# Optimization experiments

Measured on AMD Instinct MI355X. Metric: run time of the kernel, lower is better.

Reference implementation:

```python
import jax, jax.numpy as jnp
import numpy as np

N_V, N_G, K, C_IN, DW, NB, E = 8192, 4096, 128, 128, 64, 4, 65536
SIGMA, CUT = 4.0, 8.0


def setup_inputs() -> dict:
    key = jax.random.key(0)
    ks = iter(jax.random.split(key, 64))
    s = 0.05
    def rn(shape):
        return jax.random.normal(next(ks), shape, dtype=jnp.float32) * s
    p = {}
    p['vertices'] = jax.random.uniform(next(ks), (N_V, 3), dtype=jnp.float32) * 30.0
    p['graph_pos'] = jax.random.uniform(next(ks), (N_G, 3), dtype=jnp.float32) * 30.0
    p['x_in'] = jax.random.normal(next(ks), (N_V, C_IN), dtype=jnp.float32)
    p['graph_x'] = jax.random.normal(next(ks), (N_G, C_IN), dtype=jnp.float32)
    p['mass'] = jax.random.uniform(next(ks), (N_V,), dtype=jnp.float32) + 0.5
    p['evals'] = jax.random.uniform(next(ks), (K,), dtype=jnp.float32) * 10.0
    p['evecs'] = jax.random.normal(next(ks), (N_V, K), dtype=jnp.float32) * 0.011
    p['gradX'] = jax.random.normal(next(ks), (N_V, N_V), dtype=jnp.float32) * 0.01
    p['gradY'] = jax.random.normal(next(ks), (N_V, N_V), dtype=jnp.float32) * 0.01
    p['graph_edge_index'] = jax.random.randint(next(ks), (2, E), 0, N_G)
    p['graph_edge_weight'] = jax.random.uniform(next(ks), (E,), dtype=jnp.float32)
    p['lin1_w'] = rn((C_IN, DW)); p['lin1_b'] = rn((DW,))
    p['lin2_w'] = rn((C_IN, DW)); p['lin2_b'] = rn((DW,))
    p['diff_time'] = jax.random.uniform(next(ks), (NB, DW), dtype=jnp.float32) * 0.5 + 0.01
    p['A_re'] = rn((NB, DW, DW)); p['A_im'] = rn((NB, DW, DW))
    p['mlp_w0'] = rn((NB, 3 * DW, DW)); p['mlp_b0'] = rn((NB, DW))
    p['mlp_w1'] = rn((NB, DW, DW)); p['mlp_b1'] = rn((NB, DW))
    p['mlp_w2'] = rn((NB, DW, DW)); p['mlp_b2'] = rn((NB, DW))
    p['gcn1_w'] = rn((NB, DW, DW)); p['gcn1_b'] = rn((NB, DW))
    p['gcn2_w'] = rn((NB, DW, DW)); p['gcn2_b'] = rn((NB, DW))
    p['gs_w'] = rn((NB, DW, DW)); p['gs_b'] = rn((NB, DW))
    p['sg_w'] = rn((NB, DW, DW)); p['sg_b'] = rn((NB, DW))
    return p


def _gcn_conv(x, src, dst, ew, W, b, n):
    # PyG GCNConv with self-loops (fill 1.0): D^-1/2 (A+I) D^-1/2 (x W) + b
    xw = x @ W
    deg = jnp.ones((n,), xw.dtype).at[dst].add(ew)
    dinv = 1.0 / jnp.sqrt(deg)
    norm = dinv[src] * ew * dinv[dst]
    agg = jnp.zeros_like(xw).at[dst].add(norm[:, None] * xw[src])
    return agg + xw / deg[:, None] + b


def _forward(vertices, graph_pos, x_in, graph_x, mass, evals, evecs, gradX, gradY,
             graph_edge_weight, lin1_w, lin1_b, lin2_w, lin2_b, diff_time, A_re, A_im,
             mlp_w0, mlp_b0, mlp_w1, mlp_b1, mlp_w2, mlp_b2,
             gcn1_w, gcn1_b, gcn2_w, gcn2_b, gs_w, gs_b, sg_w, sg_b, graph_edge_index):
    n_v = vertices.shape[0]
    # torch.cdist + cutoff + exp(-d/sigma), under no_grad in the original
    d = jnp.sqrt(jnp.maximum(jnp.sum((vertices[:, None, :] - graph_pos[None, :, :]) ** 2, -1), 0.0))
    Wb = jax.lax.stop_gradient(jnp.where(d < CUT, jnp.exp(-d / SIGMA), 0.0))  # [n_v, n_g]
    deg_v = 1.0 + Wb.sum(1)  # vertex in-degree incl. self-loop (graphsurf direction)
    deg_g = 1.0 + Wb.sum(0)  # graph-node in-degree incl. self-loop (surfgraph direction)
    rsv = 1.0 / jnp.sqrt(deg_v)
    rsg = 1.0 / jnp.sqrt(deg_g)
    src, dst = graph_edge_index[0], graph_edge_index[1]
    diff_x = x_in @ lin1_w + lin1_b
    gx = graph_x @ lin2_w + lin2_b
    n_g = gx.shape[0]
    for i in range(NB):
        # --- DiffusionNet block (spectral) ---
        t = jnp.maximum(diff_time[i], 1e-8)
        spec = evecs.T @ (diff_x * mass[:, None])              # [K, DW]
        xd = evecs @ (jnp.exp(-evals[:, None] * t[None, :]) * spec)
        gX = gradX @ xd                                         # real part of gradient
        gY = gradY @ xd                                         # imag part of gradient
        br = gX @ A_re[i] - gY @ A_im[i]
        bi = gY @ A_re[i] + gX @ A_im[i]
        gf = jnp.tanh(gX * br + gY * bi)                        # spatial gradient features
        h = jnp.concatenate([diff_x, xd, gf], axis=-1)
        h = jax.nn.relu(h @ mlp_w0[i] + mlp_b0[i])
        h = jax.nn.relu(h @ mlp_w1[i] + mlp_b1[i])
        diff_x = diff_x + h @ mlp_w2[i] + mlp_b2[i]
        # --- internal graph GCN (eval mode: dropout = identity) ---
        gx = jax.nn.relu(_gcn_conv(gx, src, dst, graph_edge_weight, gcn1_w[i], gcn1_b[i], n_g))
        gx = _gcn_conv(gx, src, dst, graph_edge_weight, gcn2_w[i], gcn2_b[i], n_g)
        # --- bipartite GCNConvs on concatenated nodes ---
        xall = jnp.concatenate([diff_x, gx], axis=0)
        xw = xall @ gs_w[i]   # graphsurf: graph -> surface edges
        os_v = xw[:n_v] / deg_v[:, None] + (Wb @ xw[n_v:]) * rsv[:, None] + gs_b[i]
        os_g = xw[n_v:] + gs_b[i]
        xw2 = xall @ sg_w[i]  # surfgraph: surface -> graph edges
        og_g = xw2[n_v:] / deg_g[:, None] + (Wb.T @ xw2[:n_v]) * rsg[:, None] + sg_b[i]
        og_v = xw2[:n_v] + sg_b[i]
        diff_x = 0.5 * (os_v + og_v)
        gx = 0.5 * (os_g + og_g)
    return diff_x  # [n_v, C_out]


def reference(vertices, graph_pos, x_in, graph_x, mass, evals, evecs, gradX, gradY,
              graph_edge_index, graph_edge_weight, lin1_w, lin1_b, lin2_w, lin2_b,
              diff_time, A_re, A_im, mlp_w0, mlp_b0, mlp_w1, mlp_b1, mlp_w2, mlp_b2,
              gcn1_w, gcn1_b, gcn2_w, gcn2_b, gs_w, gs_b, sg_w, sg_b):
    return _forward(vertices, graph_pos, x_in, graph_x, mass, evals, evecs, gradX, gradY,
                    graph_edge_weight, lin1_w, lin1_b, lin2_w, lin2_b, diff_time, A_re, A_im,
                    mlp_w0, mlp_b0, mlp_w1, mlp_b1, mlp_w2, mlp_b2,
                    gcn1_w, gcn1_b, gcn2_w, gcn2_b, gs_w, gs_b, sg_w, sg_b, graph_edge_index)
```

## Files before the change

kernel.cpp:

```cpp
#include <hip/hip_runtime.h>
#include <hip/hip_bf16.h>

typedef unsigned short u16;
typedef __attribute__((ext_vector_type(8))) short sh8;
typedef __attribute__((ext_vector_type(4))) float f32x4;

#define NV 8192
#define NG 4096
#define NE 65536
#define NSLICE 32

__device__ __forceinline__ u16 f2bf(float f) {
  __hip_bfloat16 h = __float2bfloat16(f);
  return __builtin_bit_cast(u16, h);
}

__device__ __forceinline__ void gl_lds16(const void* g, void* l) {
  __builtin_amdgcn_global_load_lds(
      (const __attribute__((address_space(1))) void*)g,
      (__attribute__((address_space(3))) void*)l, 16, 0, 0);
}

__global__ void k_fill4(float* __restrict__ deg_v, float* __restrict__ deg_g,
                        float* __restrict__ deg_e, int* __restrict__ cnt) {
  int i = blockIdx.x * 256 + threadIdx.x;
  if (i < NV) deg_v[i] = 1.f;
  int j = i - NV;
  if (j >= 0 && j < NG) deg_g[j] = 1.f;
  j -= NG;
  if (j >= 0 && j < NG) deg_e[j] = 1.f;
  j -= NG;
  if (j >= 0 && j < NG) cnt[j] = 0;
}

__global__ __launch_bounds__(256) void k_wb_build(
    const float* __restrict__ vert, const float* __restrict__ gpos,
    u16* __restrict__ WbRow, u16* __restrict__ WbP, u16* __restrict__ WbTP,
    float* __restrict__ deg_v, float* __restrict__ deg_g) {
  __shared__ float lv[192], lg[192], colp[256];
  __shared__ float tile[64][65];
  int t = threadIdx.x;
  int v0 = blockIdx.x * 64, g0 = blockIdx.y * 64;
  if (t < 192) { lv[t] = vert[(size_t)v0 * 3 + t]; lg[t] = gpos[(size_t)g0 * 3 + t]; }
  __syncthreads();
  int w = t >> 6, lane = t & 63;
  float gx_ = lg[lane * 3], gy_ = lg[lane * 3 + 1], gz_ = lg[lane * 3 + 2];
  float csum = 0.f;
  #pragma unroll 4
  for (int s = 0; s < 16; s++) {
    int vl = w + 4 * s;
    float dx = lv[vl * 3] - gx_, dy = lv[vl * 3 + 1] - gy_, dz = lv[vl * 3 + 2] - gz_;
    float d = sqrtf(dx * dx + dy * dy + dz * dz);
    float W = (d < 8.0f) ? expf(d * -0.25f) : 0.f;
    if (WbRow != nullptr) WbRow[(size_t)(v0 + vl) * NG + g0 + lane] = f2bf(W);
    tile[vl][lane] = W;
    csum += W;
  }
  colp[t] = csum;
  __syncthreads();
  int r4 = t >> 2, q = t & 3;
  float rs = 0.f;
  #pragma unroll
  for (int j = 0; j < 16; j++) rs += tile[r4][q * 16 + j];
  rs += __shfl_xor(rs, 1);
  rs += __shfl_xor(rs, 2);
  if (q == 0) atomicAdd(&deg_v[v0 + r4], rs);
  if (w == 0) {
    float tot = colp[lane] + colp[64 + lane] + colp[128 + lane] + colp[192 + lane];
    atomicAdd(&deg_g[g0 + lane], tot);
  }
  if (WbP != nullptr) {
    size_t tb = ((size_t)(v0 >> 7) * 64 + (g0 >> 6)) * 8192;
    #pragma unroll
    for (int j = 0; j < 2; j++) {
      int idx = j * 256 + t;
      int vr = idx >> 3, k8 = (idx & 7) * 8;
      u16 pk[8];
      #pragma unroll
      for (int qq = 0; qq < 8; qq++) pk[qq] = f2bf(tile[vr][k8 + qq]);
      int r = (v0 & 64) + vr;
      *(uint4*)&WbP[tb + (size_t)r * 64 + (size_t)(((k8 >> 3) ^ (r & 7)) << 3)] = *(uint4*)pk;
    }
  }
  if (WbTP != nullptr) {
    size_t tb = ((size_t)(g0 >> 7) * 128 + (v0 >> 6)) * 8192;
    #pragma unroll
    for (int j = 0; j < 2; j++) {
      int idx = j * 256 + t;
      int gr = idx >> 3, v8 = (idx & 7) * 8;
      u16 pk[8];
      #pragma unroll
      for (int qq = 0; qq < 8; qq++) pk[qq] = f2bf(tile[v8 + qq][gr]);
      int r = (g0 & 64) + gr;
      *(uint4*)&WbTP[tb + (size_t)r * 64 + (size_t)(((v8 >> 3) ^ (r & 7)) << 3)] = *(uint4*)pk;
    }
  }
}

__global__ void k_recips(const float* __restrict__ deg_v, float* __restrict__ inv_v,
                         float* __restrict__ rs_v, const float* __restrict__ deg_g,
                         float* __restrict__ inv_g, float* __restrict__ rs_g,
                         const float* __restrict__ deg_e, float* __restrict__ inv_e,
                         float* __restrict__ rs_e) {
  int i = blockIdx.x * 256 + threadIdx.x;
  if (i < NV) { float d = deg_v[i]; inv_v[i] = 1.f / d; rs_v[i] = 1.f / sqrtf(d); }
  else if (i < NV + NG) {
    int j = i - NV; float d = deg_g[j]; inv_g[j] = 1.f / d; rs_g[j] = 1.f / sqrtf(d);
  } else if (i < NV + 2 * NG) {
    int j = i - NV - NG; float d = deg_e[j]; inv_e[j] = 1.f / d; rs_e[j] = 1.f / sqrtf(d);
  }
}

__global__ void k_edge_prep(const int* __restrict__ eidx, const float* __restrict__ ew,
                            float* __restrict__ deg_e, int* __restrict__ cnt) {
  int e = blockIdx.x * 256 + threadIdx.x;
  if (e < NE) { int d = eidx[NE + e]; atomicAdd(&deg_e[d], ew[e]); atomicAdd(&cnt[d], 1); }
}

__global__ __launch_bounds__(1024) void k_scan(const int* __restrict__ cnt,
    int* __restrict__ row_ptr, int* __restrict__ cursor) {
  __shared__ int buf0[1024], buf1[1024];
  int t = threadIdx.x;
  int b = t * 4;
  int c0 = cnt[b], c1 = cnt[b + 1], c2 = cnt[b + 2], c3 = cnt[b + 3];
  int s = c0 + c1 + c2 + c3;
  buf0[t] = s;
  __syncthreads();
  int* src = buf0; int* dst = buf1;
  for (int off = 1; off < 1024; off <<= 1) {
    int v = src[t];
    if (t >= off) v += src[t - off];
    dst[t] = v;
    __syncthreads();
    int* tmp = src; src = dst; dst = tmp;
  }
  int excl = (t == 0) ? 0 : src[t - 1];
  int r0 = excl, r1 = excl + c0, r2 = excl + c0 + c1, r3 = excl + c0 + c1 + c2;
  row_ptr[b] = r0; row_ptr[b + 1] = r1; row_ptr[b + 2] = r2; row_ptr[b + 3] = r3;
  cursor[b] = r0; cursor[b + 1] = r1; cursor[b + 2] = r2; cursor[b + 3] = r3;
  if (t == 1023) row_ptr[4096] = src[1023];
}

__global__ void k_scatter(const int* __restrict__ eidx, const float* __restrict__ ew,
                          const float* __restrict__ dinv, int* __restrict__ cursor,
                          int* __restrict__ csrc, float* __restrict__ cnorm) {
  int e = blockIdx.x * 256 + threadIdx.x;
  if (e < NE) {
    int s = eidx[e], d = eidx[NE + e];
    int slot = atomicAdd(&cursor[d], 1);
    csrc[slot] = s;
    cnorm[slot] = dinv[s] * ew[e] * dinv[d];
  }
}

__global__ __launch_bounds__(256) void k_evecsT(const float* __restrict__ ev, u16* __restrict__ evT) {
  __shared__ float tile[32][33];
  int t = threadIdx.x;
  int v0 = blockIdx.x * 32, k0 = blockIdx.y * 32;
  int r = t >> 3, c4 = (t & 7) * 4;
  float4 x = *(const float4*)(ev + (size_t)(v0 + r) * 128 + k0 + c4);
  tile[r][c4] = x.x; tile[r][c4 + 1] = x.y; tile[r][c4 + 2] = x.z; tile[r][c4 + 3] = x.w;
  __syncthreads();
  u16* dst = evT + (size_t)(k0 + r) * NV + v0 + c4;
  dst[0] = f2bf(tile[c4][r]); dst[1] = f2bf(tile[c4 + 1][r]);
  dst[2] = f2bf(tile[c4 + 2][r]); dst[3] = f2bf(tile[c4 + 3][r]);
}

__global__ __launch_bounds__(256) void gemm_setup2(
    const float* __restrict__ gXm, const float* __restrict__ gYm,
    const u16* __restrict__ evT, float* __restrict__ C2) {
  extern __shared__ __align__(16) char smem[];
  const int t = threadIdx.x;
  const int lane = t & 63, wave = t >> 6;
  const int rl = lane & 15, hi = lane >> 4;
  const int mat = blockIdx.x >> 7, mb = blockIdx.x & 127;
  const int m0 = mb * 64;
  const float* A = mat ? gYm : gXm;
  const int wm = (wave >> 1) * 32, wn = (wave & 1) * 64;

  f32x4 acc[2][4];
  #pragma unroll
  for (int a = 0; a < 2; a++)
    #pragma unroll
    for (int b = 0; b < 4; b++) acc[a][b] = f32x4{0.f, 0.f, 0.f, 0.f};

  auto STAGE = [&](int buf, int k0) {
    char* aB = smem + buf * 65536;
    #pragma unroll
    for (int jj = 0; jj < 8; jj++) {
      int j = wave * 8 + jj;
      int r = 2 * j + (lane >> 5);
      const float* src = A + (size_t)(m0 + r) * NV + k0 + (((lane & 31) ^ (r & 7)) << 2);
      gl_lds16(src, aB + j * 1024);
    }
    char* bB = aB + 32768;
    #pragma unroll
    for (int jj = 0; jj < 8; jj++) {
      int j = wave * 8 + jj;
      int n = 4 * j + (lane >> 4);
      const u16* srcb = evT + (size_t)n * NV + k0 + (((lane & 15) ^ (n & 7)) << 3);
      gl_lds16(srcb, bB + j * 1024);
    }
  };

  auto COMPUTE = [&](int buf) {
    const float* Af = (const float*)(smem + buf * 65536);
    const u16* Bf = (const u16*)(smem + buf * 65536 + 32768);
    #pragma unroll
    for (int step = 0; step < 4; step++) {
      sh8 av[2], bv[4];
      #pragma unroll
      for (int mf = 0; mf < 2; mf++) {
        int r = wm + mf * 16 + rl;
        int s0 = step * 8 + hi * 2;
        f32x4 lo = *(const f32x4*)(Af + r * 128 + ((s0 ^ (r & 7)) << 2));
        f32x4 hi4 = *(const f32x4*)(Af + r * 128 + (((s0 + 1) ^ (r & 7)) << 2));
        sh8 v;
        v[0] = (short)f2bf(lo[0]); v[1] = (short)f2bf(lo[1]);
        v[2] = (short)f2bf(lo[2]); v[3] = (short)f2bf(lo[3]);
        v[4] = (short)f2bf(hi4[0]); v[5] = (short)f2bf(hi4[1]);
        v[6] = (short)f2bf(hi4[2]); v[7] = (short)f2bf(hi4[3]);
        av[mf] = v;
      }
      #pragma unroll
      for (int nf = 0; nf < 4; nf++) {
        int n = wn + nf * 16 + rl;
        int s = step * 4 + hi;
        bv[nf] = *(const sh8*)(Bf + n * 128 + ((s ^ (n & 7)) << 3));
      }
      #pragma unroll
      for (int mf = 0; mf < 2; mf++)
        #pragma unroll
        for (int nf = 0; nf < 4; nf++)
          acc[mf][nf] = __builtin_amdgcn_mfma_f32_16x16x32_bf16(av[mf], bv[nf], acc[mf][nf], 0, 0, 0);
    }
  };

  STAGE(0, 0);
  STAGE(1, 128);
  for (int ti = 0; ti < 64; ti++) {
    if (ti + 1 < 64) { asm volatile("s_waitcnt vmcnt(16)" ::: "memory"); }
    else             { asm volatile("s_waitcnt vmcnt(0)" ::: "memory"); }
    __builtin_amdgcn_sched_barrier(0);
    __builtin_amdgcn_s_barrier();
    COMPUTE(ti & 1);
    __builtin_amdgcn_sched_barrier(0);
    __builtin_amdgcn_s_barrier();
    if (ti + 2 < 64) STAGE(ti & 1, (ti + 2) * 128);
  }

  float* C = C2 + (size_t)mat * NV * 128;
  #pragma unroll
  for (int mf = 0; mf < 2; mf++)
    #pragma unroll
    for (int nf = 0; nf < 4; nf++) {
      int row = m0 + wm + mf * 16 + hi * 4;
      int col = wn + nf * 16 + rl;
      #pragma unroll
      for (int q = 0; q < 4; q++)
        C[(size_t)(row + q) * 128 + col] = acc[mf][nf][q];
    }
}

__global__ __launch_bounds__(256) void gemm_panel(
    const u16* __restrict__ Apan, int KT, const u16* __restrict__ BT, int ldbt,
    float* __restrict__ parts, int M, int nz, int ktpz) {
  __shared__ __align__(16) char smem[49152];
  const int t = threadIdx.x;
  const int lane = t & 63, wave = t >> 6;
  const int rl = lane & 15, hi = lane >> 4;
  const int mb = blockIdx.x / nz, z = blockIdx.x % nz;
  const int kt0 = z * ktpz;
  const int wm = wave * 32;

  f32x4 acc[2][4];
  #pragma unroll
  for (int a = 0; a < 2; a++)
    #pragma unroll
    for (int b = 0; b < 4; b++) acc[a][b] = f32x4{0.f, 0.f, 0.f, 0.f};

  auto STAGE = [&](int buf, int kt) {
    char* aB = smem + buf * 24576;
    const u16* tbase = Apan + ((size_t)mb * KT + kt) * 8192;
    #pragma unroll
    for (int jj = 0; jj < 4; jj++) {
      int j = wave * 4 + jj;
      gl_lds16(tbase + j * 512 + lane * 8, aB + j * 1024);
    }
    char* bB = aB + 16384;
    #pragma unroll
    for (int jj = 0; jj < 2; jj++) {
      int j = wave * 2 + jj;
      int n = 8 * j + (lane >> 3);
      const u16* srcb = BT + (size_t)n * ldbt + kt * 64 + (((lane & 7) ^ (n & 7)) << 3);
      gl_lds16(srcb, bB + j * 1024);
    }
  };

  auto COMPUTE = [&](int buf) {
    const u16* Af = (const u16*)(smem + buf * 24576);
    const u16* Bf = Af + 8192;
    #pragma unroll
    for (int step = 0; step < 2; step++) {
      sh8 av[2], bv[4];
      int s = step * 4 + hi;
      #pragma unroll
      for (int mf = 0; mf < 2; mf++) {
        int r = wm + mf * 16 + rl;
        av[mf] = *(const sh8*)(Af + r * 64 + ((s ^ (r & 7)) << 3));
      }
      #pragma unroll
      for (int nf = 0; nf < 4; nf++) {
        int n = nf * 16 + rl;
        bv[nf] = *(const sh8*)(Bf + n * 64 + ((s ^ (n & 7)) << 3));
      }
      #pragma unroll
      for (int mf = 0; mf < 2; mf++)
        #pragma unroll
        for (int nf = 0; nf < 4; nf++)
          acc[mf][nf] = __builtin_amdgcn_mfma_f32_16x16x32_bf16(av[mf], bv[nf], acc[mf][nf], 0, 0, 0);
    }
  };

  STAGE(0, kt0);
  if (ktpz > 1) STAGE(1, kt0 + 1);
  for (int ti = 0; ti < ktpz; ti++) {
    if (ti + 1 < ktpz) { asm volatile("s_waitcnt vmcnt(6)" ::: "memory"); }
    else               { asm volatile("s_waitcnt vmcnt(0)" ::: "memory"); }
    __builtin_amdgcn_sched_barrier(0);
    __builtin_amdgcn_s_barrier();
    COMPUTE(ti & 1);
    __builtin_amdgcn_sched_barrier(0);
    __builtin_amdgcn_s_barrier();
    if (ti + 2 < ktpz) STAGE(ti & 1, kt0 + ti + 2);
  }

  float* C = parts + (size_t)z * M * 64;
  #pragma unroll
  for (int mf = 0; mf < 2; mf++)
    #pragma unroll
    for (int nf = 0; nf < 4; nf++) {
      int row = mb * 128 + wm + mf * 16 + hi * 4;
      int col = nf * 16 + rl;
      #pragma unroll
      for (int q = 0; q < 4; q++)
        C[(size_t)(row + q) * 64 + col] = acc[mf][nf][q];
    }
}

__global__ __launch_bounds__(256) void gemm_bf16(
    const u16* __restrict__ Ab, int lda, const u16* __restrict__ BT, int ldbt,
    float* __restrict__ parts, int M, int kchunk) {
  __shared__ __align__(16) char smem[49152];
  const int t = threadIdx.x;
  const int lane = t & 63, wave = t >> 6;
  const int m0 = blockIdx.x * 128;
  const int kbeg = blockIdx.z * kchunk;
  const int nt = kchunk >> 6;
  const int wm = (wave >> 1) * 64, wn = (wave & 1) * 32;
  const int arl = lane >> 3, asl = lane & 7;

  f32x4 acc[4][2];
  #pragma unroll
  for (int a = 0; a < 4; a++)
    #pragma unroll
    for (int b = 0; b < 2; b++) acc[a][b] = f32x4{0.f, 0.f, 0.f, 0.f};

  auto STAGE = [&](int buf, int k0) {
    char* base = smem + buf * 24576;
    #pragma unroll
    for (int j = 0; j < 4; j++) {
      int R0 = (wave * 4 + j) * 8;
      int r = R0 + arl;
      int gs = asl ^ (r & 7);
      gl_lds16(Ab + (size_t)(m0 + r) * lda + k0 + gs * 8, base + R0 * 128);
    }
    char* bb = base + 16384;
    #pragma unroll
    for (int j = 0; j < 2; j++) {
      int R0 = (wave * 2 + j) * 8;
      int r = R0 + arl;
      int gs = asl ^ (r & 7);
      gl_lds16(BT + (size_t)r * ldbt + k0 + gs * 8, bb + R0 * 128);
    }
  };

  auto COMPUTE = [&](int buf) {
    char* base = smem + buf * 24576;
    const u16* Af = (const u16*)base;
    const u16* Bf = (const u16*)(base + 16384);
    #pragma unroll
    for (int kk = 0; kk < 2; kk++) {
      sh8 av[4], bv[2];
      #pragma unroll
      for (int mf = 0; mf < 4; mf++) {
        int r = wm + mf * 16 + (lane & 15);
        int g = kk * 4 + (lane >> 4);
        av[mf] = *(const sh8*)(Af + r * 64 + (g ^ (r & 7)) * 8);
      }
      #pragma unroll
      for (int nf = 0; nf < 2; nf++) {
        int r = wn + nf * 16 + (lane & 15);
        int g = kk * 4 + (lane >> 4);
        bv[nf] = *(const sh8*)(Bf + r * 64 + (g ^ (r & 7)) * 8);
      }
      #pragma unroll
      for (int mf = 0; mf < 4; mf++)
        #pragma unroll
        for (int nf = 0; nf < 2; nf++)
          acc[mf][nf] = __builtin_amdgcn_mfma_f32_16x16x32_bf16(av[mf], bv[nf], acc[mf][nf], 0, 0, 0);
    }
  };

  STAGE(0, kbeg);
  if (nt > 1) STAGE(1, kbeg + 64);
  for (int ti = 0; ti < nt; ti++) {
    if (ti + 1 < nt) { asm volatile("s_waitcnt vmcnt(6)" ::: "memory"); }
    else             { asm volatile("s_waitcnt vmcnt(0)" ::: "memory"); }
    __builtin_amdgcn_sched_barrier(0);
    __builtin_amdgcn_s_barrier();
    COMPUTE(ti & 1);
    __builtin_amdgcn_sched_barrier(0);
    __builtin_amdgcn_s_barrier();
    if (ti + 2 < nt) STAGE(ti & 1, kbeg + (ti + 2) * 64);
  }

  float* C = parts + (size_t)blockIdx.z * M * 64;
  #pragma unroll
  for (int mf = 0; mf < 4; mf++)
    #pragma unroll
    for (int nf = 0; nf < 2; nf++) {
      int row = m0 + wm + mf * 16 + (lane >> 4) * 4;
      int col = wn + nf * 16 + (lane & 15);
      #pragma unroll
      for (int q = 0; q < 4; q++)
        C[(size_t)(row + q) * 64 + col] = acc[mf][nf][q];
    }
}

template<int BN, bool AF32, bool ATRANS>
__global__ __launch_bounds__(256) void gemm_k(
    const void* __restrict__ Aptr, const void* __restrict__ A2, int zsplit2,
    const u16* __restrict__ BT, float* __restrict__ Cpart,
    int M, int N, int lda, int ldbt, int kchunk) {
  constexpr int NF = BN / 32;
  __shared__ u16 lA[128 * 40];
  __shared__ u16 lB[BN * 40];
  const int t = threadIdx.x;
  const int m0 = blockIdx.x * 128, n0 = blockIdx.y * BN;
  const void* Ause = Aptr;
  int kz = blockIdx.z;
  if (A2 != nullptr && kz >= zsplit2) { Ause = A2; kz -= zsplit2; }
  const int kbeg = kz * kchunk;
  const int lane = t & 63, wave = t >> 6;
  const int wm = (wave >> 1) * 64, wn = (wave & 1) * (BN / 2);
  f32x4 zero = {0.f, 0.f, 0.f, 0.f};
  f32x4 acc[4][NF];
  #pragma unroll
  for (int a = 0; a < 4; a++)
    #pragma unroll
    for (int b = 0; b < NF; b++) acc[a][b] = zero;

  for (int k0 = kbeg; k0 < kbeg + kchunk; k0 += 32) {
    if constexpr (!ATRANS) {
      const int r = t >> 1, cc = (t & 1) * 16;
      const u16* A = (const u16*)Ause + (size_t)(m0 + r) * lda + k0 + cc;
      *(uint4*)&lA[r * 40 + cc] = *(const uint4*)A;
      *(uint4*)&lA[r * 40 + cc + 8] = *(const uint4*)(A + 8);
    } else {
      const int kl = t >> 3, mb = (t & 7) * 16;
      const u16* A = (const u16*)Ause + (size_t)(k0 + kl) * lda + m0 + mb;
      u16 vals[16];
      *(uint4*)&vals[0] = *(const uint4*)A;
      *(uint4*)&vals[8] = *(const uint4*)(A + 8);
      #pragma unroll
      for (int j = 0; j < 16; j++) lA[(mb + j) * 40 + kl] = vals[j];
    }
    if constexpr (BN == 64) {
      const int r = t >> 2, cc = (t & 3) * 8;
      const u16* B = BT + (size_t)(n0 + r) * ldbt + k0 + cc;
      *(uint4*)&lB[r * 40 + cc] = *(const uint4*)B;
    } else {
      const int r = t >> 1, cc = (t & 1) * 16;
      const u16* B = BT + (size_t)(n0 + r) * ldbt + k0 + cc;
      *(uint4*)&lB[r * 40 + cc] = *(const uint4*)B;
      *(uint4*)&lB[r * 40 + cc + 8] = *(const uint4*)(B + 8);
    }
    __syncthreads();
    sh8 af[4], bfv[NF];
    #pragma unroll
    for (int mf = 0; mf < 4; mf++)
      af[mf] = *(const sh8*)&lA[(wm + mf * 16 + (lane & 15)) * 40 + (lane >> 4) * 8];
    #pragma unroll
    for (int nf = 0; nf < NF; nf++)
      bfv[nf] = *(const sh8*)&lB[(wn + nf * 16 + (lane & 15)) * 40 + (lane >> 4) * 8];
    #pragma unroll
    for (int mf = 0; mf < 4; mf++)
      #pragma unroll
      for (int nf = 0; nf < NF; nf++)
        acc[mf][nf] = __builtin_amdgcn_mfma_f32_16x16x32_bf16(af[mf], bfv[nf], acc[mf][nf], 0, 0, 0);
    __syncthreads();
  }
  float* C = Cpart + (size_t)blockIdx.z * M * N;
  #pragma unroll
  for (int mf = 0; mf < 4; mf++)
    #pragma unroll
    for (int nf = 0; nf < NF; nf++) {
      const int row = m0 + wm + mf * 16 + (lane >> 4) * 4;
      const int col = n0 + wn + nf * 16 + (lane & 15);
      #pragma unroll
      for (int q = 0; q < 4; q++)
        C[(size_t)(row + q) * N + col] = acc[mf][nf][q];
    }
}

__global__ void k_reduce(const float* __restrict__ parts, float* __restrict__ dst, int len, int nz) {
  int i = (blockIdx.x * 256 + threadIdx.x) * 4;
  if (i >= len) return;
  float4 s = *(const float4*)(parts + i);
  for (int z = 1; z < nz; z++) {
    float4 v = *(const float4*)(parts + (size_t)z * len + i);
    s.x += v.x; s.y += v.y; s.z += v.z; s.w += v.w;
  }
  *(float4*)(dst + i) = s;
}

__global__ __launch_bounds__(256) void k_lin_both(const float* __restrict__ x_in,
    const float* __restrict__ graph_x, const float* __restrict__ W1,
    const float* __restrict__ b1, const float* __restrict__ W2,
    const float* __restrict__ b2, float* __restrict__ outV, float* __restrict__ outG) {
  __shared__ float lW[8192];
  __shared__ float lb[64];
  int bb = blockIdx.x;
  bool isV = bb < 2048;
  const float* W = isV ? W1 : W2;
  const float* bi = isV ? b1 : b2;
  const float* A = isV ? x_in : graph_x;
  float* out = isV ? outV : outG;
  int rb = isV ? bb : bb - 2048;
  int t = threadIdx.x;
  for (int i = t; i < 8192; i += 256) lW[i] = W[i];
  if (t < 64) lb[t] = bi[t];
  __syncthreads();
  int row = rb * 4 + (t >> 6), c = t & 63;
  const float* Ar = A + (size_t)row * 128;
  float acc = lb[c];
  #pragma unroll 8
  for (int k = 0; k < 128; k++) acc += Ar[k] * lW[k * 64 + c];
  out[(size_t)row * 64 + c] = acc;
}

__global__ __launch_bounds__(64) void k_spec_part(const float* __restrict__ evecs,
    const float* __restrict__ mass, const float* __restrict__ dx, float* __restrict__ sp) {
  int k = blockIdx.x, c = threadIdx.x;
  int v0 = blockIdx.y * 256;
  float a0 = 0, a1 = 0, a2 = 0, a3 = 0;
  for (int v = v0; v < v0 + 256; v += 4) {
    a0 += evecs[(size_t)(v + 0) * 128 + k] * mass[v + 0] * dx[(size_t)(v + 0) * 64 + c];
    a1 += evecs[(size_t)(v + 1) * 128 + k] * mass[v + 1] * dx[(size_t)(v + 1) * 64 + c];
    a2 += evecs[(size_t)(v + 2) * 128 + k] * mass[v + 2] * dx[(size_t)(v + 2) * 64 + c];
    a3 += evecs[(size_t)(v + 3) * 128 + k] * mass[v + 3] * dx[(size_t)(v + 3) * 64 + c];
  }
  sp[(size_t)blockIdx.y * 8192 + k * 64 + c] = (a0 + a1) + (a2 + a3);
}

__global__ void k_es(const float* __restrict__ sp, const float* __restrict__ evals,
                     const float* __restrict__ dt, float* __restrict__ Es) {
  int i = blockIdx.x * 256 + threadIdx.x;
  int k = i >> 6, c = i & 63;
  float s = 0.f;
  #pragma unroll 8
  for (int z = 0; z < NSLICE; z++) s += sp[(size_t)z * 8192 + i];
  Es[i] = expf(-evals[k] * fmaxf(dt[c], 1e-8f)) * s;
}

__global__ __launch_bounds__(256) void k_xdgf(const float* __restrict__ evecs,
    const float* __restrict__ GXE, const float* __restrict__ GYE,
    const float* __restrict__ Es, const float* __restrict__ Are,
    const float* __restrict__ Aim, float* __restrict__ xd, float* __restrict__ gf) {
  __shared__ float lE[8192];
  __shared__ float lr[4096], li[4096];
  __shared__ float lgx[256], lgy[256];
  int t = threadIdx.x;
  for (int i = t; i < 8192; i += 256) lE[i] = Es[i];
  for (int i = t; i < 4096; i += 256) { lr[i] = Are[i]; li[i] = Aim[i]; }
  __syncthreads();
  int wr = t >> 6, c = t & 63;
  int row = blockIdx.x * 4 + wr;
  const float* er = evecs + (size_t)row * 128;
  const float* xr = GXE + (size_t)row * 128;
  const float* yr = GYE + (size_t)row * 128;
  float a0 = 0, a1 = 0, a2 = 0;
  #pragma unroll 8
  for (int k = 0; k < 128; k++) {
    float s = lE[k * 64 + c];
    a0 += er[k] * s; a1 += xr[k] * s; a2 += yr[k] * s;
  }
  lgx[wr * 64 + c] = a1;
  lgy[wr * 64 + c] = a2;
  __syncthreads();
  float br = 0.f, bi = 0.f;
  #pragma unroll 8
  for (int k = 0; k < 64; k++) {
    float gx = lgx[wr * 64 + k], gy = lgy[wr * 64 + k];
    float ar = lr[k * 64 + c], ai = li[k * 64 + c];
    br += gx * ar - gy * ai;
    bi += gy * ar + gx * ai;
  }
  xd[(size_t)row * 64 + c] = a0;
  gf[(size_t)row * 64 + c] = tanhf(a1 * br + a2 * bi);
}

__global__ __launch_bounds__(256) void k_mlp0(const float* __restrict__ dx,
    const float* __restrict__ xd, const float* __restrict__ gf,
    const float* __restrict__ W0, const float* __restrict__ b0, float* __restrict__ h1) {
  __shared__ float lW[12288];
  __shared__ float lb[64];
  int t = threadIdx.x;
  for (int i = t; i < 12288; i += 256) lW[i] = W0[i];
  if (t < 64) lb[t] = b0[t];
  __syncthreads();
  int row = blockIdx.x * 4 + (t >> 6), c = t & 63;
  const float* a0 = dx + (size_t)row * 64;
  const float* a1 = xd + (size_t)row * 64;
  const float* a2 = gf + (size_t)row * 64;
  float acc = lb[c];
  #pragma unroll 8
  for (int k = 0; k < 64; k++) acc += a0[k] * lW[k * 64 + c];
  #pragma unroll 8
  for (int k = 0; k < 64; k++) acc += a1[k] * lW[(64 + k) * 64 + c];
  #pragma unroll 8
  for (int k = 0; k < 64; k++) acc += a2[k] * lW[(128 + k) * 64 + c];
  h1[(size_t)row * 64 + c] = fmaxf(acc, 0.f);
}

__global__ __launch_bounds__(256) void k_mlp12(const float* __restrict__ h1,
    const float* __restrict__ W1, const float* __restrict__ b1,
    const float* __restrict__ W2, const float* __restrict__ b2, float* __restrict__ dx) {
  __shared__ float l1[4096], l2[4096], lb1[64], lb2[64], lrow[256];
  int t = threadIdx.x;
  for (int i = t; i < 4096; i += 256) { l1[i] = W1[i]; l2[i] = W2[i]; }
  if (t < 64) lb1[t] = b1[t];
  else if (t < 128) lb2[t - 64] = b2[t - 64];
  __syncthreads();
  int wr = t >> 6, c = t & 63;
  int row = blockIdx.x * 4 + wr;
  const float* hr = h1 + (size_t)row * 64;
  float h2 = lb1[c];
  #pragma unroll 8
  for (int k = 0; k < 64; k++) h2 += hr[k] * l1[k * 64 + c];
  h2 = fmaxf(h2, 0.f);
  lrow[wr * 64 + c] = h2;
  __syncthreads();
  float o = lb2[c] + dx[(size_t)row * 64 + c];
  #pragma unroll 8
  for (int k = 0; k < 64; k++) o += lrow[wr * 64 + k] * l2[k * 64 + c];
  dx[(size_t)row * 64 + c] = o;
}

template<bool BIAS, bool RELU, bool RES>
__global__ __launch_bounds__(256) void k_mm64(const float* __restrict__ A,
    const float* __restrict__ W, const float* __restrict__ b,
    const float* __restrict__ res, float* __restrict__ out) {
  __shared__ float lW[4096];
  __shared__ float lb[64];
  int t = threadIdx.x;
  for (int i = t; i < 4096; i += 256) lW[i] = W[i];
  if constexpr (BIAS) { if (t < 64) lb[t] = b[t]; }
  __syncthreads();
  int row = blockIdx.x * 4 + (t >> 6), c = t & 63;
  const float* Ar = A + (size_t)row * 64;
  float acc = 0.f;
  #pragma unroll 8
  for (int k = 0; k < 64; k++) acc += Ar[k] * lW[k * 64 + c];
  if constexpr (BIAS) acc += lb[c];
  if constexpr (RES) acc += res[(size_t)row * 64 + c];
  if constexpr (RELU) acc = fmaxf(acc, 0.f);
  out[(size_t)row * 64 + c] = acc;
}

template<bool TP, bool TQ>
__global__ __launch_bounds__(256) void k_mm_dual(const float* __restrict__ A,
    const float* __restrict__ W1, const float* __restrict__ W2,
    float* __restrict__ P, float* __restrict__ Q,
    u16* __restrict__ PT, u16* __restrict__ QT, int R) {
  __shared__ float l1[4096], l2[4096];
  int t = threadIdx.x;
  for (int i = t; i < 4096; i += 256) { l1[i] = W1[i]; l2[i] = W2[i]; }
  __syncthreads();
  int row = blockIdx.x * 4 + (t >> 6), c = t & 63;
  const float* Ar = A + (size_t)row * 64;
  float p = 0.f, q = 0.f;
  #pragma unroll 8
  for (int k = 0; k < 64; k++) { float a = Ar[k]; p += a * l1[k * 64 + c]; q += a * l2[k * 64 + c]; }
  P[(size_t)row * 64 + c] = p;
  Q[(size_t)row * 64 + c] = q;
  if constexpr (TP) PT[(size_t)c * R + row] = f2bf(p);
  if constexpr (TQ) QT[(size_t)c * R + row] = f2bf(q);
}

__global__ __launch_bounds__(64) void k_aggmm(const float* __restrict__ xw,
    const int* __restrict__ rp, const int* __restrict__ csrc,
    const float* __restrict__ cnorm, const float* __restrict__ invdeg,
    const float* __restrict__ b1, const float* __restrict__ W2, float* __restrict__ out) {
  __shared__ float lrow[64];
  int g = blockIdx.x, c = threadIdx.x;
  float acc = xw[(size_t)g * 64 + c] * invdeg[g] + b1[c];
  int j1 = rp[g + 1];
  for (int j = rp[g]; j < j1; j++) acc += cnorm[j] * xw[(size_t)csrc[j] * 64 + c];
  acc = fmaxf(acc, 0.f);
  lrow[c] = acc;
  __syncthreads();
  float o = 0.f;
  #pragma unroll 8
  for (int k = 0; k < 64; k++) o += lrow[k] * W2[k * 64 + c];
  out[(size_t)g * 64 + c] = o;
}

__global__ __launch_bounds__(64) void k_aggdual(const float* __restrict__ xw,
    const int* __restrict__ rp, const int* __restrict__ csrc,
    const float* __restrict__ cnorm, const float* __restrict__ invdeg,
    const float* __restrict__ b2, const float* __restrict__ gsw,
    const float* __restrict__ sgw, float* __restrict__ xw_g,
    float* __restrict__ xw2_g, u16* __restrict__ xwgT) {
  __shared__ float lrow[64];
  int g = blockIdx.x, c = threadIdx.x;
  float acc = xw[(size_t)g * 64 + c] * invdeg[g] + b2[c];
  int j1 = rp[g + 1];
  for (int j = rp[g]; j < j1; j++) acc += cnorm[j] * xw[(size_t)csrc[j] * 64 + c];
  lrow[c] = acc;
  __syncthreads();
  float p = 0.f, q = 0.f;
  #pragma unroll 8
  for (int k = 0; k < 64; k++) {
    float r = lrow[k];
    p += r * gsw[k * 64 + c];
    q += r * sgw[k * 64 + c];
  }
  xw_g[(size_t)g * 64 + c] = p;
  xw2_g[(size_t)g * 64 + c] = q;
  xwgT[(size_t)c * NG + g] = f2bf(p);
}

__global__ void k_combine(const float* __restrict__ xw_v, const float* __restrict__ Wbp,
    const float* __restrict__ xw2_v, const float* __restrict__ xw_g,
    const float* __restrict__ WbTp, const float* __restrict__ xw2_g,
    const float* __restrict__ inv_deg_v, const float* __restrict__ rsv,
    const float* __restrict__ inv_deg_g, const float* __restrict__ rsg,
    const float* __restrict__ gsb, const float* __restrict__ sgb,
    float* __restrict__ dx, float* __restrict__ gx) {
  int idx = blockIdx.x * 256 + threadIdx.x;
  if (idx < NV * 64) {
    int v = idx >> 6, c = idx & 63;
    dx[idx] = 0.5f * (xw_v[idx] * inv_deg_v[v] + Wbp[idx] * rsv[v] + gsb[c] + xw2_v[idx] + sgb[c]);
  } else {
    int j = idx - NV * 64;
    int g = j >> 6, c = j & 63;
    gx[j] = 0.5f * (xw_g[j] + gsb[c] + xw2_g[j] * inv_deg_g[g] + WbTp[j] * rsg[g] + sgb[c]);
  }
}

extern "C" void kernel_launch(void* const* d_in, const int* in_sizes, int n_in,
                              void* d_out, int out_size, void* d_ws, size_t ws_size,
                              hipStream_t stream) {
  const float* vertices  = (const float*)d_in[0];
  const float* graph_pos = (const float*)d_in[1];
  const float* x_in      = (const float*)d_in[2];
  const float* graph_x   = (const float*)d_in[3];
  const float* mass      = (const float*)d_in[4];
  const float* evals     = (const float*)d_in[5];
  const float* evecs     = (const float*)d_in[6];
  const float* gradX     = (const float*)d_in[7];
  const float* gradY     = (const float*)d_in[8];
  const int*   eidx      = (const int*)d_in[9];
  const float* ew        = (const float*)d_in[10];
  const float* lin1_w    = (const float*)d_in[11];
  const float* lin1_b    = (const float*)d_in[12];
  const float* lin2_w    = (const float*)d_in[13];
  const float* lin2_b    = (const float*)d_in[14];
  const float* diff_time = (const float*)d_in[15];
  const float* A_re      = (const float*)d_in[16];
  const float* A_im      = (const float*)d_in[17];
  const float* mlp_w0    = (const float*)d_in[18];
  const float* mlp_b0    = (const float*)d_in[19];
  const float* mlp_w1    = (const float*)d_in[20];
  const float* mlp_b1    = (const float*)d_in[21];
  const float* mlp_w2    = (const float*)d_in[22];
  const float* mlp_b2    = (const float*)d_in[23];
  const float* gcn1_w    = (const float*)d_in[24];
  const float* gcn1_b    = (const float*)d_in[25];
  const float* gcn2_w    = (const float*)d_in[26];
  const float* gcn2_b    = (const float*)d_in[27];
  const float* gs_w      = (const float*)d_in[28];
  const float* gs_b      = (const float*)d_in[29];
  const float* sg_w      = (const float*)d_in[30];
  const float* sg_b      = (const float*)d_in[31];

  char* base = (char*)d_ws;
  size_t off = 0;
  auto alloc = [&](size_t nbytes) -> void* {
    void* p = base + off;
    off += (nbytes + 255) & ~(size_t)255;
    return p;
  };
  const size_t MBy = 1024 * 1024;
  u16*   evecsT  = (u16*)alloc((size_t)128 * NV * 2);
  float* GXE2    = (float*)alloc((size_t)2 * NV * 128 * 4);
  float* GXE     = GXE2;
  float* GYE     = GXE2 + (size_t)NV * 128;
  float* sp      = (float*)alloc((size_t)NSLICE * 8192 * 4);
  float* Es      = (float*)alloc(8192 * 4);
  float* diffx   = (float*)alloc((size_t)NV * 64 * 4);
  float* gxb     = (float*)alloc((size_t)NG * 64 * 4);
  float* xd      = (float*)alloc((size_t)NV * 64 * 4);
  float* gf      = (float*)alloc((size_t)NV * 64 * 4);
  float* h1      = (float*)alloc((size_t)NV * 64 * 4);
  float* xw_v    = (float*)alloc((size_t)NV * 64 * 4);
  float* xw2_v   = (float*)alloc((size_t)NV * 64 * 4);
  float* xw_g    = (float*)alloc((size_t)NG * 64 * 4);
  float* xw2_g   = (float*)alloc((size_t)NG * 64 * 4);
  float* xw1     = (float*)alloc((size_t)NG * 64 * 4);
  float* xw2k    = (float*)alloc((size_t)NG * 64 * 4);
  u16*   xwgT    = (u16*)alloc((size_t)64 * NG * 2);
  u16*   xw2vT   = (u16*)alloc((size_t)64 * NV * 2);
  float* Wbp     = (float*)alloc((size_t)NV * 64 * 4);
  float* WbTp    = (float*)alloc((size_t)NG * 64 * 4);
  float* deg_v   = (float*)alloc(NV * 4);
  float* inv_deg_v = (float*)alloc(NV * 4);
  float* rsv     = (float*)alloc(NV * 4);
  float* deg_g   = (float*)alloc(NG * 4);
  float* inv_deg_g = (float*)alloc(NG * 4);
  float* rsg     = (float*)alloc(NG * 4);
  float* deg_e   = (float*)alloc(NG * 4);
  float* invdeg_e = (float*)alloc(NG * 4);
  float* dinv_e  = (float*)alloc(NG * 4);
  int*   cnt     = (int*)alloc(NG * 4);
  int*   row_ptr = (int*)alloc((NG + 1) * 4);
  int*   cursor  = (int*)alloc(NG * 4);
  int*   csr_src = (int*)alloc(NE * 4);
  float* csr_norm = (float*)alloc(NE * 4);

  size_t avail = ws_size > off ? ws_size - off : 0;
  u16 *WbP = nullptr, *WbTP = nullptr, *WbRow = nullptr;
  float* parts;
  if (avail >= 146 * MBy) {
    WbP  = (u16*)alloc((size_t)NV * NG * 2);
    WbTP = (u16*)alloc((size_t)NG * NV * 2);
    parts = (float*)alloc(16 * MBy);
  } else if (avail >= 81 * MBy) {
    WbRow = (u16*)alloc((size_t)NV * NG * 2);
    parts = (float*)alloc(16 * MBy);
  } else {
    WbRow = (u16*)alloc((size_t)NV * NG * 2);
    parts = (float*)alloc(16 * MBy);
  }
  if (off > ws_size) return;

  dim3 B256(256);

  k_fill4<<<dim3(80), B256, 0, stream>>>(deg_v, deg_g, deg_e, cnt);
  k_wb_build<<<dim3(128, 64), B256, 0, stream>>>(vertices, graph_pos, WbRow, WbP, WbTP, deg_v, deg_g);
  k_edge_prep<<<dim3(256), B256, 0, stream>>>(eidx, ew, deg_e, cnt);
  k_recips<<<dim3(64), B256, 0, stream>>>(deg_v, inv_deg_v, rsv, deg_g, inv_deg_g, rsg,
                                          deg_e, invdeg_e, dinv_e);
  k_scan<<<dim3(1), dim3(1024), 0, stream>>>(cnt, row_ptr, cursor);
  k_scatter<<<dim3(256), B256, 0, stream>>>(eidx, ew, dinv_e, cursor, csr_src, csr_norm);
  k_evecsT<<<dim3(256, 4), B256, 0, stream>>>(evecs, evecsT);
  gemm_setup2<<<dim3(256), B256, 131072, stream>>>(gradX, gradY, evecsT, GXE2);
  k_lin_both<<<dim3(3072), B256, 0, stream>>>(x_in, graph_x, lin1_w, lin1_b, lin2_w, lin2_b, diffx, gxb);

  for (int i = 0; i < 4; i++) {
    const float* dtrow = diff_time + i * 64;
    k_spec_part<<<dim3(128, NSLICE), dim3(64), 0, stream>>>(evecs, mass, diffx, sp);
    k_es<<<dim3(32), B256, 0, stream>>>(sp, evals, dtrow, Es);
    k_xdgf<<<dim3(2048), B256, 0, stream>>>(evecs, GXE, GYE, Es, A_re + i * 4096, A_im + i * 4096, xd, gf);
    k_mlp0<<<dim3(2048), B256, 0, stream>>>(diffx, xd, gf, mlp_w0 + i * 12288, mlp_b0 + i * 64, h1);
    k_mlp12<<<dim3(2048), B256, 0, stream>>>(h1, mlp_w1 + i * 4096, mlp_b1 + i * 64,
        mlp_w2 + i * 4096, mlp_b2 + i * 64, diffx);
    k_mm64<false, false, false><<<dim3(1024), B256, 0, stream>>>(gxb, gcn1_w + i * 4096, nullptr, nullptr, xw1);
    k_aggmm<<<dim3(NG), dim3(64), 0, stream>>>(xw1, row_ptr, csr_src, csr_norm, invdeg_e,
        gcn1_b + i * 64, gcn2_w + i * 4096, xw2k);
    k_aggdual<<<dim3(NG), dim3(64), 0, stream>>>(xw2k, row_ptr, csr_src, csr_norm, invdeg_e,
        gcn2_b + i * 64, gs_w + i * 4096, sg_w + i * 4096, xw_g, xw2_g, xwgT);
    k_mm_dual<false, true><<<dim3(2048), B256, 0, stream>>>(diffx, gs_w + i * 4096, sg_w + i * 4096,
        xw_v, xw2_v, nullptr, xw2vT, NV);
    if (WbP != nullptr) {
      gemm_panel<<<dim3(64 * 8), B256, 0, stream>>>(WbP, 64, xwgT, NG, parts, NV, 8, 8);
      k_reduce<<<dim3(512), B256, 0, stream>>>(parts, Wbp, NV * 64, 8);
      gemm_panel<<<dim3(32 * 16), B256, 0, stream>>>(WbTP, 128, xw2vT, NV, parts, NG, 16, 8);
      k_reduce<<<dim3(256), B256, 0, stream>>>(parts, WbTp, NG * 64, 16);
    } else {
      gemm_bf16<<<dim3(64, 1, 8), B256, 0, stream>>>(WbRow, NG, xwgT, NG, parts, NV, 512);
      k_reduce<<<dim3(512), B256, 0, stream>>>(parts, Wbp, NV * 64, 8);
      gemm_k<64, false, true><<<dim3(32, 1, 16), B256, 0, stream>>>(
          WbRow, nullptr, 1 << 30, xw2vT, parts, NG, 64, NG, NV, 512);
      k_reduce<<<dim3(256), B256, 0, stream>>>(parts, WbTp, NG * 64, 16);
    }
    k_combine<<<dim3(3072), B256, 0, stream>>>(xw_v, Wbp, xw2_v, xw_g, WbTp, xw2_g,
        inv_deg_v, rsv, inv_deg_g, rsg, gs_b + i * 64, sg_b + i * 64, diffx, gxb);
  }

  hipMemcpyAsync(d_out, diffx, (size_t)NV * 64 * 4, hipMemcpyDeviceToDevice, stream);
}
```

Baseline: 1.070 ms.

## Split-K setup GEMM with larger tiles; move spectral projection onto MFMA GEMM

The setup GEMM (gradX/gradY times evecs) is rebuilt with 256x128 tiles and K=32 stages, split across zsu K-chunks, and its partial results are summed by a new reduce kernel. The intent is better MFMA reuse and more blocks in flight for a GEMM that is bound by fp32 streaming. The per-block spectral projection, previously a scalar fp32 loop over 32 slices, now transposes mass*diffx into bf16 and runs the existing gemm_bf16 with 64-way split-K plus a reduce. This adds kernel launches, partial-sum traffic, more workspace, and bf16 rounding in the spectral coefficients.

```diff
diff --git a/kernel.cpp b/kernel.cpp
--- a/kernel.cpp
+++ b/kernel.cpp
@@ -8,7 +8,6 @@
 #define NV 8192
 #define NG 4096
 #define NE 65536
-#define NSLICE 32
 
 __device__ __forceinline__ u16 f2bf(float f) {
   __hip_bfloat16 h = __float2bfloat16(f);
@@ -166,96 +165,122 @@
   dst[2] = f2bf(tile[c4 + 2][r]); dst[3] = f2bf(tile[c4 + 3][r]);
 }
 
-__global__ __launch_bounds__(256) void gemm_setup2(
+__global__ __launch_bounds__(256) void k_mdxT(const float* __restrict__ dx,
+    const float* __restrict__ mass, u16* __restrict__ mdxT) {
+  __shared__ float tile[64][65];
+  __shared__ float lm[64];
+  int t = threadIdx.x;
+  int v0 = blockIdx.x * 64;
+  if (t < 64) lm[t] = mass[v0 + t];
+  #pragma unroll
+  for (int i = 0; i < 16; i++) {
+    int idx = i * 256 + t;
+    int r = idx >> 6, c = idx & 63;
+    tile[r][c] = dx[(size_t)(v0 + r) * 64 + c];
+  }
+  __syncthreads();
+  int c = t >> 2;
+  #pragma unroll
+  for (int i = 0; i < 2; i++) {
+    int vq = (t & 3) * 16 + i * 8;
+    u16 pk[8];
+    #pragma unroll
+    for (int q = 0; q < 8; q++) pk[q] = f2bf(lm[vq + q] * tile[vq + q][c]);
+    *(uint4*)&mdxT[(size_t)c * NV + v0 + vq] = *(uint4*)pk;
+  }
+}
+
+__global__ __launch_bounds__(256) void gemm_setup3(
     const float* __restrict__ gXm, const float* __restrict__ gYm,
-    const u16* __restrict__ evT, float* __restrict__ C2) {
+    const u16* __restrict__ evT, float* __restrict__ parts,
+    int z, int kchunk) {
   extern __shared__ __align__(16) char smem[];
   const int t = threadIdx.x;
   const int lane = t & 63, wave = t >> 6;
   const int rl = lane & 15, hi = lane >> 4;
-  const int mat = blockIdx.x >> 7, mb = blockIdx.x & 127;
-  const int m0 = mb * 64;
+  int b = blockIdx.x;
+  const int zi = b % z; b /= z;
+  const int mb = b & 31;
+  const int mat = b >> 5;
   const float* A = mat ? gYm : gXm;
-  const int wm = (wave >> 1) * 32, wn = (wave & 1) * 64;
-
-  f32x4 acc[2][4];
-  #pragma unroll
-  for (int a = 0; a < 2; a++)
-    #pragma unroll
-    for (int b = 0; b < 4; b++) acc[a][b] = f32x4{0.f, 0.f, 0.f, 0.f};
+  const int m0 = mb * 256;
+  const int kbeg = zi * kchunk;
+  const int nt = kchunk >> 5;
+  const int wm = wave * 64;
+
+  f32x4 acc[4][8];
+  #pragma unroll
+  for (int a = 0; a < 4; a++)
+    #pragma unroll
+    for (int bb = 0; bb < 8; bb++) acc[a][bb] = f32x4{0.f, 0.f, 0.f, 0.f};
 
   auto STAGE = [&](int buf, int k0) {
-    char* aB = smem + buf * 65536;
+    char* aB = smem + buf * 40960;
     #pragma unroll
     for (int jj = 0; jj < 8; jj++) {
-      int j = wave * 8 + jj;
-      int r = 2 * j + (lane >> 5);
-      const float* src = A + (size_t)(m0 + r) * NV + k0 + (((lane & 31) ^ (r & 7)) << 2);
-      gl_lds16(src, aB + j * 1024);
-    }
-    char* bB = aB + 32768;
-    #pragma unroll
-    for (int jj = 0; jj < 8; jj++) {
-      int j = wave * 8 + jj;
-      int n = 4 * j + (lane >> 4);
-      const u16* srcb = evT + (size_t)n * NV + k0 + (((lane & 15) ^ (n & 7)) << 3);
-      gl_lds16(srcb, bB + j * 1024);
+      int R0 = wave * 64 + jj * 8;
+      int r = R0 + (lane >> 3);
+      int s = lane & 7;
+      gl_lds16(A + (size_t)(m0 + r) * NV + k0 + ((s ^ (r & 7)) << 2), aB + R0 * 128);
+    }
+    char* bB = smem + buf * 40960 + 32768;
+    #pragma unroll
+    for (int jj = 0; jj < 2; jj++) {
+      int R0 = wave * 32 + jj * 16;
+      int n = R0 + (lane >> 2);
+      int s = lane & 3;
+      gl_lds16(evT + (size_t)n * NV + k0 + ((s ^ ((n >> 1) & 3)) << 3), bB + R0 * 64);
     }
   };
 
   auto COMPUTE = [&](int buf) {
-    const float* Af = (const float*)(smem + buf * 65536);
-    const u16* Bf = (const u16*)(smem + buf * 65536 + 32768);
-    #pragma unroll
-    for (int step = 0; step < 4; step++) {
-      sh8 av[2], bv[4];
-      #pragma unroll
-      for (int mf = 0; mf < 2; mf++) {
-        int r = wm + mf * 16 + rl;
-        int s0 = step * 8 + hi * 2;
-        f32x4 lo = *(const f32x4*)(Af + r * 128 + ((s0 ^ (r & 7)) << 2));
-        f32x4 hi4 = *(const f32x4*)(Af + r * 128 + (((s0 + 1) ^ (r & 7)) << 2));
-        sh8 v;
-        v[0] = (short)f2bf(lo[0]); v[1] = (short)f2bf(lo[1]);
-        v[2] = (short)f2bf(lo[2]); v[3] = (short)f2bf(lo[3]);
-        v[4] = (short)f2bf(hi4[0]); v[5] = (short)f2bf(hi4[1]);
-        v[6] = (short)f2bf(hi4[2]); v[7] = (short)f2bf(hi4[3]);
-        av[mf] = v;
-      }
-      #pragma unroll
-      for (int nf = 0; nf < 4; nf++) {
-        int n = wn + nf * 16 + rl;
-        int s = step * 4 + hi;
-        bv[nf] = *(const sh8*)(Bf + n * 128 + ((s ^ (n & 7)) << 3));
-      }
-      #pragma unroll
-      for (int mf = 0; mf < 2; mf++)
-        #pragma unroll
-        for (int nf = 0; nf < 4; nf++)
-          acc[mf][nf] = __builtin_amdgcn_mfma_f32_16x16x32_bf16(av[mf], bv[nf], acc[mf][nf], 0, 0, 0);
-    }
+    const float* Af = (const float*)(smem + buf * 40960);
+    const u16* Bf = (const u16*)(smem + buf * 40960 + 32768);
+    sh8 av[4], bv[8];
+    #pragma unroll
+    for (int mf = 0; mf < 4; mf++) {
+      int r = wm + mf * 16 + rl;
+      f32x4 lo = *(const f32x4*)(Af + r * 32 + (((2 * hi) ^ (r & 7)) << 2));
+      f32x4 h4 = *(const f32x4*)(Af + r * 32 + (((2 * hi + 1) ^ (r & 7)) << 2));
+      sh8 v;
+      v[0] = (short)f2bf(lo[0]); v[1] = (short)f2bf(lo[1]);
+      v[2] = (short)f2bf(lo[2]); v[3] = (short)f2bf(lo[3]);
+      v[4] = (short)f2bf(h4[0]); v[5] = (short)f2bf(h4[1]);
+      v[6] = (short)f2bf(h4[2]); v[7] = (short)f2bf(h4[3]);
+      av[mf] = v;
+    }
+    #pragma unroll
+    for (int nf = 0; nf < 8; nf++) {
+      int n = nf * 16 + rl;
+      bv[nf] = *(const sh8*)(Bf + n * 32 + ((hi ^ ((n >> 1) & 3)) << 3));
+    }
+    #pragma unroll
+    for (int mf = 0; mf < 4; mf++)
+      #pragma unroll
+      for (int nf = 0; nf < 8; nf++)
+        acc[mf][nf] = __builtin_amdgcn_mfma_f32_16x16x32_bf16(av[mf], bv[nf], acc[mf][nf], 0, 0, 0);
   };
 
-  STAGE(0, 0);
-  STAGE(1, 128);
-  for (int ti = 0; ti < 64; ti++) {
-    if (ti + 1 < 64) { asm volatile("s_waitcnt vmcnt(16)" ::: "memory"); }
+  STAGE(0, kbeg);
+  if (nt > 1) STAGE(1, kbeg + 32);
+  for (int ti = 0; ti < nt; ti++) {
+    if (ti + 1 < nt) { asm volatile("s_waitcnt vmcnt(10)" ::: "memory"); }
     else             { asm volatile("s_waitcnt vmcnt(0)" ::: "memory"); }
     __builtin_amdgcn_sched_barrier(0);
     __builtin_amdgcn_s_barrier();
     COMPUTE(ti & 1);
     __builtin_amdgcn_sched_barrier(0);
     __builtin_amdgcn_s_barrier();
-    if (ti + 2 < 64) STAGE(ti & 1, (ti + 2) * 128);
-  }
-
-  float* C = C2 + (size_t)mat * NV * 128;
-  #pragma unroll
-  for (int mf = 0; mf < 2; mf++)
-    #pragma unroll
-    for (int nf = 0; nf < 4; nf++) {
+    if (ti + 2 < nt) STAGE(ti & 1, kbeg + (ti + 2) * 32);
+  }
+
+  float* C = parts + (size_t)(mat * z + zi) * (NV * 128);
+  #pragma unroll
+  for (int mf = 0; mf < 4; mf++)
+    #pragma unroll
+    for (int nf = 0; nf < 8; nf++) {
       int row = m0 + wm + mf * 16 + hi * 4;
-      int col = wn + nf * 16 + rl;
+      int col = nf * 16 + rl;
       #pragma unroll
       for (int q = 0; q < 4; q++)
         C[(size_t)(row + q) * 128 + col] = acc[mf][nf][q];
@@ -525,6 +550,19 @@
   *(float4*)(dst + i) = s;
 }
 
+__global__ void k_reduce2(const float* __restrict__ parts, float* __restrict__ dst, int len, int nz) {
+  int i = (blockIdx.x * 256 + threadIdx.x) * 4;
+  if (i >= 2 * len) return;
+  int mat = i / len, j = i - mat * len;
+  const float* src = parts + (size_t)mat * nz * len + j;
+  float4 s = *(const float4*)src;
+  for (int z = 1; z < nz; z++) {
+    float4 v = *(const float4*)(src + (size_t)z * len);
+    s.x += v.x; s.y += v.y; s.z += v.z; s.w += v.w;
+  }
+  *(float4*)(dst + i) = s;
+}
+
 __global__ __launch_bounds__(256) void k_lin_both(const float* __restrict__ x_in,
     const float* __restrict__ graph_x, const float* __restrict__ W1,
     const float* __restrict__ b1, const float* __restrict__ W2,
@@ -550,28 +588,11 @@
   out[(size_t)row * 64 + c] = acc;
 }
 
-__global__ __launch_bounds__(64) void k_spec_part(const float* __restrict__ evecs,
-    const float* __restrict__ mass, const float* __restrict__ dx, float* __restrict__ sp) {
-  int k = blockIdx.x, c = threadIdx.x;
-  int v0 = blockIdx.y * 256;
-  float a0 = 0, a1 = 0, a2 = 0, a3 = 0;
-  for (int v = v0; v < v0 + 256; v += 4) {
-    a0 += evecs[(size_t)(v + 0) * 128 + k] * mass[v + 0] * dx[(size_t)(v + 0) * 64 + c];
-    a1 += evecs[(size_t)(v + 1) * 128 + k] * mass[v + 1] * dx[(size_t)(v + 1) * 64 + c];
-    a2 += evecs[(size_t)(v + 2) * 128 + k] * mass[v + 2] * dx[(size_t)(v + 2) * 64 + c];
-    a3 += evecs[(size_t)(v + 3) * 128 + k] * mass[v + 3] * dx[(size_t)(v + 3) * 64 + c];
-  }
-  sp[(size_t)blockIdx.y * 8192 + k * 64 + c] = (a0 + a1) + (a2 + a3);
-}
-
-__global__ void k_es(const float* __restrict__ sp, const float* __restrict__ evals,
+__global__ void k_es(const float* __restrict__ specsum, const float* __restrict__ evals,
                      const float* __restrict__ dt, float* __restrict__ Es) {
   int i = blockIdx.x * 256 + threadIdx.x;
   int k = i >> 6, c = i & 63;
-  float s = 0.f;
-  #pragma unroll 8
-  for (int z = 0; z < NSLICE; z++) s += sp[(size_t)z * 8192 + i];
-  Es[i] = expf(-evals[k] * fmaxf(dt[c], 1e-8f)) * s;
+  Es[i] = expf(-evals[k] * fmaxf(dt[c], 1e-8f)) * specsum[i];
 }
 
 __global__ __launch_bounds__(256) void k_xdgf(const float* __restrict__ evecs,
@@ -808,7 +829,8 @@
   float* GXE2    = (float*)alloc((size_t)2 * NV * 128 * 4);
   float* GXE     = GXE2;
   float* GYE     = GXE2 + (size_t)NV * 128;
-  float* sp      = (float*)alloc((size_t)NSLICE * 8192 * 4);
+  u16*   mdxT    = (u16*)alloc((size_t)64 * NV * 2);
+  float* spec    = (float*)alloc(8192 * 4);
   float* Es      = (float*)alloc(8192 * 4);
   float* diffx   = (float*)alloc((size_t)NV * 64 * 4);
   float* gxb     = (float*)alloc((size_t)NG * 64 * 4);
@@ -843,16 +865,20 @@
   size_t avail = ws_size > off ? ws_size - off : 0;
   u16 *WbP = nullptr, *WbTP = nullptr, *WbRow = nullptr;
   float* parts;
-  if (avail >= 146 * MBy) {
+  int zsu;
+  if (avail >= 162 * MBy) {
     WbP  = (u16*)alloc((size_t)NV * NG * 2);
     WbTP = (u16*)alloc((size_t)NG * NV * 2);
-    parts = (float*)alloc(16 * MBy);
-  } else if (avail >= 81 * MBy) {
+    parts = (float*)alloc(32 * MBy);
+    zsu = 4;
+  } else if (avail >= 97 * MBy) {
     WbRow = (u16*)alloc((size_t)NV * NG * 2);
-    parts = (float*)alloc(16 * MBy);
+    parts = (float*)alloc(32 * MBy);
+    zsu = 4;
   } else {
     WbRow = (u16*)alloc((size_t)NV * NG * 2);
     parts = (float*)alloc(16 * MBy);
+    zsu = 2;
   }
   if (off > ws_size) return;
 
@@ -866,13 +892,17 @@
   k_scan<<<dim3(1), dim3(1024), 0, stream>>>(cnt, row_ptr, cursor);
   k_scatter<<<dim3(256), B256, 0, stream>>>(eidx, ew, dinv_e, cursor, csr_src, csr_norm);
   k_evecsT<<<dim3(256, 4), B256, 0, stream>>>(evecs, evecsT);
-  gemm_setup2<<<dim3(256), B256, 131072, stream>>>(gradX, gradY, evecsT, GXE2);
+  gemm_setup3<<<dim3(2 * 32 * zsu), B256, 81920, stream>>>(
+      gradX, gradY, evecsT, parts, zsu, 8192 / zsu);
+  k_reduce2<<<dim3(2048), B256, 0, stream>>>(parts, GXE2, NV * 128, zsu);
   k_lin_both<<<dim3(3072), B256, 0, stream>>>(x_in, graph_x, lin1_w, lin1_b, lin2_w, lin2_b, diffx, gxb);
 
   for (int i = 0; i < 4; i++) {
     const float* dtrow = diff_time + i * 64;
-    k_spec_part<<<dim3(128, NSLICE), dim3(64), 0, stream>>>(evecs, mass, diffx, sp);
-    k_es<<<dim3(32), B256, 0, stream>>>(sp, evals, dtrow, Es);
+    k_mdxT<<<dim3(128), B256, 0, stream>>>(diffx, mass, mdxT);
+    gemm_bf16<<<dim3(1, 1, 64), B256, 0, stream>>>(evecsT, NV, mdxT, NV, parts, 128, 128);
+    k_reduce<<<dim3(8), B256, 0, stream>>>(parts, spec, 8192, 64);
+    k_es<<<dim3(32), B256, 0, stream>>>(spec, evals, dtrow, Es);
     k_xdgf<<<dim3(2048), B256, 0, stream>>>(evecs, GXE, GYE, Es, A_re + i * 4096, A_im + i * 4096, xd, gf);
     k_mlp0<<<dim3(2048), B256, 0, stream>>>(diffx, xd, gf, mlp_w0 + i * 12288, mlp_b0 + i * 64, h1);
     k_mlp12<<<dim3(2048), B256, 0, stream>>>(h1, mlp_w1 + i * 4096, mlp_b1 + i * 64,
```

Result: faster. 1.036 ms (-3.2%).
